# Kernel optimization log

Measured on AMD Instinct MI355X. Metric: run time of the kernel, lower is better.

Reference implementation:

```python
import jax, jax.numpy as jnp
import numpy as np

N_ITERS = 10
ETA = 0.1


def setup_inputs() -> dict:
    key = jax.random.key(0)
    k1, k2, k3 = jax.random.split(key, 3)
    u = jax.random.normal(k1, (65536, 512), dtype=jnp.float32)
    G_raw = jax.random.normal(k2, (512, 512), dtype=jnp.float32) * 0.01
    # log_lam initialized as log(0.5), matching lam_init=0.5
    log_lam = jnp.asarray(np.log(0.5), dtype=jnp.float32)
    return {"u": u, "G_raw": G_raw, "log_lam": log_lam}


def reference(u, G_raw, log_lam):
    lam = jnp.exp(log_lam)
    # symmetrize and zero the diagonal
    G = 0.5 * (G_raw + G_raw.T)
    G = G - jnp.diag(jnp.diagonal(G))

    def step(carry, _):
        v, a = carry
        dv = u - v - a @ G          # [N, dim]
        v = v + ETA * dv
        a = jnp.sign(v) * jax.nn.relu(jnp.abs(v) - lam)  # soft threshold
        return (v, a), None

    init = (jnp.zeros_like(u), jnp.zeros_like(u))
    (v, a), _ = jax.lax.scan(step, init, None, length=N_ITERS)
    return a
```

## Files before the change

### kernel.cpp

```cpp
#include <hip/hip_runtime.h>
#include <hip/hip_bf16.h>


typedef __attribute__((ext_vector_type(8))) short bf16x8;
typedef __attribute__((ext_vector_type(16))) float f32x16;

#define ETA 0.1f

__device__ __forceinline__ unsigned short f2bf(float f) {
  union { float f; unsigned u; } x; x.f = f;
  unsigned r = x.u + 0x7fffu + ((x.u >> 16) & 1u);
  return (unsigned short)(r >> 16);
}

__global__ void prep_G(const float* __restrict__ Graw, unsigned short* __restrict__ Gb) {
  int idx = blockIdx.x * blockDim.x + threadIdx.x;
  int k = idx >> 9, n = idx & 511;
  float g = 0.5f * (Graw[k * 512 + n] + Graw[n * 512 + k]);
  if (k == n) g = 0.f;
  int kk = k >> 4, ct = n >> 5;
  int lane = (n & 31) + (((k >> 3) & 1) << 5);
  int j = k & 7;
  Gb[((((kk * 16 + ct) * 64) + lane) << 3) + j] = f2bf(g);
}

__global__ __launch_bounds__(512, 2) void lca_kernel(
    const float* __restrict__ u_g, const unsigned short* __restrict__ Gb,
    const float* __restrict__ log_lam, float* __restrict__ out) {
  __shared__ unsigned short sA[64 * 520];

  const int tid = threadIdx.x;
  const int lane = tid & 63;
  const int wave = tid >> 6;
  const int R0 = blockIdx.x * 64;
  const int cl = lane & 31;
  const int rquad = (lane >> 5) * 4;
  const int C0 = wave * 64;

  const float lam = expf(log_lam[0]);

  f32x16 acc[2][2];
  f32x16 uu[2][2];

  #pragma unroll
  for (int rt = 0; rt < 2; ++rt) {
    #pragma unroll
    for (int ctl = 0; ctl < 2; ++ctl) {
      const float* base = u_g + (R0 + rt * 32 + rquad) * 512 + C0 + ctl * 32 + cl;
      f32x16 t;
      #pragma unroll
      for (int reg = 0; reg < 16; ++reg) {
        const int rofs = (reg & 3) + 8 * (reg >> 2);
        t[reg] = base[rofs * 512];
      }
      uu[rt][ctl] = t;
      acc[rt][ctl] = -t;
    }
  }

  auto epilogue = [&]() {
    #pragma unroll
    for (int rt = 0; rt < 2; ++rt) {
      #pragma unroll
      for (int ctl = 0; ctl < 2; ++ctl) {
        unsigned short* sa = &sA[(rt * 32 + rquad) * 520 + C0 + ctl * 32 + cl];
        #pragma unroll
        for (int reg = 0; reg < 16; ++reg) {
          const int rofs = (reg & 3) + 8 * (reg >> 2);
          float v = -ETA * acc[rt][ctl][reg];
          float av = copysignf(fmaxf(fabsf(v) - lam, 0.f), v);
          sa[rofs * 520] = f2bf(av);
        }
        acc[rt][ctl] = 0.9f * acc[rt][ctl] - uu[rt][ctl];
      }
    }
  };

  epilogue();
  __syncthreads();

  const unsigned short* paRow = sA + cl * 520 + ((lane >> 5) << 3);
  const bf16x8* gb = (const bf16x8*)Gb;
  const int bbase = wave * 2 * 64 + lane;

  #pragma unroll 1
  for (int t = 1; t < 10; ++t) {
    #pragma unroll 4
    for (int kk = 0; kk < 32; ++kk) {
      bf16x8 a0 = *(const bf16x8*)(paRow + kk * 16);
      bf16x8 a1 = *(const bf16x8*)(paRow + 32 * 520 + kk * 16);
      bf16x8 b0 = gb[bbase + kk * 1024];
      bf16x8 b1 = gb[bbase + kk * 1024 + 64];
      acc[0][0] = __builtin_amdgcn_mfma_f32_32x32x16_bf16(a0, b0, acc[0][0], 0, 0, 0);
      acc[0][1] = __builtin_amdgcn_mfma_f32_32x32x16_bf16(a0, b1, acc[0][1], 0, 0, 0);
      acc[1][0] = __builtin_amdgcn_mfma_f32_32x32x16_bf16(a1, b0, acc[1][0], 0, 0, 0);
      acc[1][1] = __builtin_amdgcn_mfma_f32_32x32x16_bf16(a1, b1, acc[1][1], 0, 0, 0);
    }
    __syncthreads();
    if (t < 9) {
      epilogue();
      __syncthreads();
    }
  }

  #pragma unroll
  for (int rt = 0; rt < 2; ++rt) {
    #pragma unroll
    for (int ctl = 0; ctl < 2; ++ctl) {
      float* ob = out + (R0 + rt * 32 + rquad) * 512 + C0 + ctl * 32 + cl;
      #pragma unroll
      for (int reg = 0; reg < 16; ++reg) {
        const int rofs = (reg & 3) + 8 * (reg >> 2);
        float v = -ETA * acc[rt][ctl][reg];
        ob[rofs * 512] = copysignf(fmaxf(fabsf(v) - lam, 0.f), v);
      }
    }
  }
}

extern "C" void kernel_launch(void* const* d_in, const int* in_sizes, int n_in,
                              void* d_out, int out_size, void* d_ws, size_t ws_size,
                              hipStream_t stream) {
  const float* u = (const float*)d_in[0];
  const float* Graw = (const float*)d_in[1];
  const float* log_lam = (const float*)d_in[2];
  float* out = (float*)d_out;
  unsigned short* Gb = (unsigned short*)d_ws;

  prep_G<<<dim3(1024), dim3(256), 0, stream>>>(Graw, Gb);
  lca_kernel<<<dim3(1024), dim3(512), 0, stream>>>(u, Gb, log_lam, out);
}
```

Measured before the change: 539.7 us.

## Reload u from global each iteration to cut registers and double occupancy

```diff
diff --git a/kernel.cpp b/kernel.cpp
--- a/kernel.cpp
+++ b/kernel.cpp
@@ -9,8 +9,7 @@
 
 __device__ __forceinline__ unsigned short f2bf(float f) {
   union { float f; unsigned u; } x; x.f = f;
-  unsigned r = x.u + 0x7fffu + ((x.u >> 16) & 1u);
-  return (unsigned short)(r >> 16);
+  return (unsigned short)((x.u + 0x8000u) >> 16);
 }
 
 __global__ void prep_G(const float* __restrict__ Graw, unsigned short* __restrict__ Gb) {
@@ -24,7 +23,7 @@
   Gb[((((kk * 16 + ct) * 64) + lane) << 3) + j] = f2bf(g);
 }
 
-__global__ __launch_bounds__(512, 2) void lca_kernel(
+__global__ __launch_bounds__(512, 4) void lca_kernel(
     const float* __restrict__ u_g, const unsigned short* __restrict__ Gb,
     const float* __restrict__ log_lam, float* __restrict__ out) {
   __shared__ unsigned short sA[64 * 520];
@@ -40,43 +39,29 @@
   const float lam = expf(log_lam[0]);
 
   f32x16 acc[2][2];
-  f32x16 uu[2][2];
 
   #pragma unroll
   for (int rt = 0; rt < 2; ++rt) {
     #pragma unroll
     for (int ctl = 0; ctl < 2; ++ctl) {
-      const float* base = u_g + (R0 + rt * 32 + rquad) * 512 + C0 + ctl * 32 + cl;
-      f32x16 t;
+      const float* ub = u_g + (R0 + rt * 32 + rquad) * 512 + C0 + ctl * 32 + cl;
+      unsigned short* sa = &sA[(rt * 32 + rquad) * 520 + C0 + ctl * 32 + cl];
+      f32x16 tu;
       #pragma unroll
       for (int reg = 0; reg < 16; ++reg) {
         const int rofs = (reg & 3) + 8 * (reg >> 2);
-        t[reg] = base[rofs * 512];
+        tu[reg] = ub[rofs * 512];
       }
-      uu[rt][ctl] = t;
-      acc[rt][ctl] = -t;
+      #pragma unroll
+      for (int reg = 0; reg < 16; ++reg) {
+        const int rofs = (reg & 3) + 8 * (reg >> 2);
+        float v = ETA * tu[reg];
+        float c = __builtin_amdgcn_fmed3f(v, -lam, lam);
+        sa[rofs * 520] = f2bf(v - c);
+        acc[rt][ctl][reg] = -1.9f * tu[reg];
+      }
     }
   }
-
-  auto epilogue = [&]() {
-    #pragma unroll
-    for (int rt = 0; rt < 2; ++rt) {
-      #pragma unroll
-      for (int ctl = 0; ctl < 2; ++ctl) {
-        unsigned short* sa = &sA[(rt * 32 + rquad) * 520 + C0 + ctl * 32 + cl];
-        #pragma unroll
-        for (int reg = 0; reg < 16; ++reg) {
-          const int rofs = (reg & 3) + 8 * (reg >> 2);
-          float v = -ETA * acc[rt][ctl][reg];
-          float av = copysignf(fmaxf(fabsf(v) - lam, 0.f), v);
-          sa[rofs * 520] = f2bf(av);
-        }
-        acc[rt][ctl] = 0.9f * acc[rt][ctl] - uu[rt][ctl];
-      }
-    }
-  };
-
-  epilogue();
   __syncthreads();
 
   const unsigned short* paRow = sA + cl * 520 + ((lane >> 5) << 3);
@@ -98,7 +83,28 @@
     }
     __syncthreads();
     if (t < 9) {
-      epilogue();
+      #pragma unroll
+      for (int rt = 0; rt < 2; ++rt) {
+        #pragma unroll
+        for (int ctl = 0; ctl < 2; ++ctl) {
+          const float* ub = u_g + (R0 + rt * 32 + rquad) * 512 + C0 + ctl * 32 + cl;
+          unsigned short* sa = &sA[(rt * 32 + rquad) * 520 + C0 + ctl * 32 + cl];
+          f32x16 tu;
+          #pragma unroll
+          for (int reg = 0; reg < 16; ++reg) {
+            const int rofs = (reg & 3) + 8 * (reg >> 2);
+            tu[reg] = ub[rofs * 512];
+          }
+          #pragma unroll
+          for (int reg = 0; reg < 16; ++reg) {
+            const int rofs = (reg & 3) + 8 * (reg >> 2);
+            float v = -ETA * acc[rt][ctl][reg];
+            float c = __builtin_amdgcn_fmed3f(v, -lam, lam);
+            sa[rofs * 520] = f2bf(v - c);
+            acc[rt][ctl][reg] = 0.9f * acc[rt][ctl][reg] - tu[reg];
+          }
+        }
+      }
       __syncthreads();
     }
   }
@@ -112,7 +118,8 @@
       for (int reg = 0; reg < 16; ++reg) {
         const int rofs = (reg & 3) + 8 * (reg >> 2);
         float v = -ETA * acc[rt][ctl][reg];
-        ob[rofs * 512] = copysignf(fmaxf(fabsf(v) - lam, 0.f), v);
+        float c = __builtin_amdgcn_fmed3f(v, -lam, lam);
+        ob[rofs * 512] = v - c;
       }
     }
   }
```

Result: slower. 754.3 us (+39.8%).
